# Optimization experiments

Hardware: AMD Instinct MI355X
Metric: run time of the kernel (lower is better)

Reference implementation:

```python
import jax, jax.numpy as jnp
import numpy as np

H_SIZE = 1024
N_HEADS = 16
D_K = H_SIZE // N_HEADS


def setup_inputs() -> dict:
    key = jax.random.key(0)
    ks = jax.random.split(key, 12)
    s = 1.0 / np.sqrt(H_SIZE)
    inp = {
        "x": jax.random.normal(ks[0], (2, 2048, H_SIZE), dtype=jnp.float32),
        "Wq": jax.random.uniform(ks[1], (H_SIZE, H_SIZE), minval=-s, maxval=s),
        "bq": jax.random.uniform(ks[2], (H_SIZE,), minval=-s, maxval=s),
        "Wk": jax.random.uniform(ks[3], (H_SIZE, H_SIZE), minval=-s, maxval=s),
        "bk": jax.random.uniform(ks[4], (H_SIZE,), minval=-s, maxval=s),
        "Wv": jax.random.uniform(ks[5], (H_SIZE, H_SIZE), minval=-s, maxval=s),
        "bv": jax.random.uniform(ks[6], (H_SIZE,), minval=-s, maxval=s),
        "Wo": jax.random.uniform(ks[7], (H_SIZE, H_SIZE), minval=-s, maxval=s),
        "bo": jax.random.uniform(ks[8], (H_SIZE,), minval=-s, maxval=s),
        "ln_gamma": jnp.ones((H_SIZE,), dtype=jnp.float32),
        "ln_beta": jnp.zeros((H_SIZE,), dtype=jnp.float32),
    }
    return inp


def reference(x, Wq, bq, Wk, bk, Wv, bv, Wo, bo, ln_gamma, ln_beta):
    B, L, H = x.shape
    residual = x
    # QKV projections -> [B, n_heads, L, d_k]
    def proj(W, b):
        return (x @ W.T + b).reshape(B, L, N_HEADS, D_K).transpose(0, 2, 1, 3)
    q = proj(Wq, bq)
    k = proj(Wk, bk)
    v = proj(Wv, bv)
    # scaled dot-product attention (dropout = identity in eval mode)
    scores = jnp.einsum("bhqd,bhkd->bhqk", q, k) / jnp.sqrt(jnp.float32(D_K))
    attn = jax.nn.softmax(scores, axis=-1)
    out = jnp.einsum("bhqk,bhkd->bhqd", attn, v)
    out = out.transpose(0, 2, 1, 3).reshape(B, L, H)
    out = out @ Wo.T + bo
    # residual + LayerNorm
    y = out + residual
    mu = jnp.mean(y, axis=-1, keepdims=True)
    var = jnp.var(y, axis=-1, keepdims=True)
    y = (y - mu) / jnp.sqrt(var + 1e-5) * ln_gamma + ln_beta
    return y
```

## Files before the change

### kernel.cpp

```cpp
#include <hip/hip_runtime.h>

#define H_SIZE 1024
#define N_HEADS 16
#define D_K 64
#define SEQ 2048
#define BATCH 2
#define M_TOT 4096

typedef __bf16 __attribute__((ext_vector_type(8))) bf16_8;
typedef float __attribute__((ext_vector_type(4))) f32x4;
typedef float __attribute__((ext_vector_type(16))) f32x16;
typedef int __attribute__((ext_vector_type(4))) int4v;

__device__ __forceinline__ ushort f2bf(float f) {
    unsigned int u = __float_as_uint(f);
    unsigned int r = (u + 0x7FFFu + ((u >> 16) & 1u)) >> 16;
    return (ushort)r;
}

__device__ __forceinline__ unsigned int cvtpk(float lo, float hi) {
    unsigned int r;
    asm("v_cvt_pk_bf16_f32 %0, %1, %2" : "=v"(r) : "v"(lo), "v"(hi));
    return r;
}

__device__ __forceinline__ void gld16(void* lds, const void* g) {
    __builtin_amdgcn_global_load_lds(
        (const __attribute__((address_space(1))) unsigned int*)g,
        (__attribute__((address_space(3))) unsigned int*)lds, 16, 0, 0);
}

__global__ __launch_bounds__(256) void cast_all_kernel(
    const float* __restrict__ x, const float* __restrict__ wq, const float* __restrict__ wk,
    const float* __restrict__ wv, const float* __restrict__ wo,
    ushort* __restrict__ xb, ushort* __restrict__ wqb, ushort* __restrict__ wkb,
    ushort* __restrict__ wvb, ushort* __restrict__ wob) {
    int i = blockIdx.x * 256 + threadIdx.x;
    const float* src;
    ushort* dst;
    int off;
    if (i < 1048576) {
        src = x; dst = xb; off = i;
    } else {
        int j = i - 1048576;
        int w = j >> 18;
        off = j & 262143;
        src = (w == 0) ? wq : (w == 1) ? wk : (w == 2) ? wv : wo;
        dst = (w == 0) ? wqb : (w == 1) ? wkb : (w == 2) ? wvb : wob;
    }
    float4 v = ((const float4*)src)[off];
    ushort4 o;
    o.x = f2bf(v.x); o.y = f2bf(v.y); o.z = f2bf(v.z); o.w = f2bf(v.w);
    ((ushort4*)dst)[off] = o;
}

__global__ __launch_bounds__(256) void gemm_qkv(
    const ushort* __restrict__ A, const ushort* __restrict__ wq,
    const ushort* __restrict__ wk, const ushort* __restrict__ wv,
    const float* __restrict__ bq, const float* __restrict__ bk, const float* __restrict__ bv,
    ushort* __restrict__ Qb, ushort* __restrict__ Kb, ushort* __restrict__ Vtb) {
    constexpr int LDST = 40;
    __shared__ ushort As[2][128 * LDST];
    __shared__ ushort Bs[2][128 * LDST];
    const int tid = threadIdx.x;
    const int lane = tid & 63, wid = tid >> 6;
    const int wr = wid >> 1, wc = wid & 1;
    const int hi = lane >> 4, lo = lane & 15;
    const int bm0 = blockIdx.x * 128;
    const int t3 = blockIdx.y >> 3;
    const int bn0 = (blockIdx.y & 7) * 128;
    const ushort* Bw = (t3 == 0) ? wq : (t3 == 1) ? wk : wv;
    const float* bias = (t3 == 0) ? bq : (t3 == 1) ? bk : bv;

    f32x4 acc[4][4] = {};

    const int r = tid >> 1, c0 = (tid & 1) * 16;
    const ushort* ga = A + (size_t)(bm0 + r) * H_SIZE + c0;
    const ushort* gb = Bw + (size_t)(bn0 + r) * H_SIZE + c0;

    int4v a0, a1, b0, b1;
#define LOADR(kt)                                  \
    {                                              \
        a0 = *(const int4v*)(ga + (kt));           \
        a1 = *(const int4v*)(ga + (kt) + 8);       \
        b0 = *(const int4v*)(gb + (kt));           \
        b1 = *(const int4v*)(gb + (kt) + 8);       \
    }
#define STORER(bb)                                 \
    {                                              \
        ushort* sa = &As[bb][r * LDST + c0];       \
        *(int4v*)sa = a0; *(int4v*)(sa + 8) = a1;  \
        ushort* sb = &Bs[bb][r * LDST + c0];       \
        *(int4v*)sb = b0; *(int4v*)(sb + 8) = b1;  \
    }

    LOADR(0);
    STORER(0);
    __syncthreads();
    int cur = 0;
    constexpr int NT = H_SIZE / 32;
    for (int t = 0; t < NT; t++) {
        if (t + 1 < NT) LOADR((t + 1) * 32);
        {
            bf16_8 af[4], bfv[4];
            const ushort* pa = &As[cur][(wr * 64 + lo) * LDST + hi * 8];
            const ushort* pb = &Bs[cur][(wc * 64 + lo) * LDST + hi * 8];
#pragma unroll
            for (int i = 0; i < 4; i++) af[i] = *(const bf16_8*)(pa + i * 16 * LDST);
#pragma unroll
            for (int i = 0; i < 4; i++) bfv[i] = *(const bf16_8*)(pb + i * 16 * LDST);
#pragma unroll
            for (int mi = 0; mi < 4; mi++)
#pragma unroll
                for (int ni = 0; ni < 4; ni++)
                    acc[mi][ni] = __builtin_amdgcn_mfma_f32_16x16x32_bf16(
                        af[mi], bfv[ni], acc[mi][ni], 0, 0, 0);
        }
        if (t + 1 < NT) {
            STORER(cur ^ 1);
            __syncthreads();
        }
        cur ^= 1;
    }
#undef LOADR
#undef STORER

#pragma unroll
    for (int mi = 0; mi < 4; mi++) {
#pragma unroll
        for (int ni = 0; ni < 4; ni++) {
            const int row0 = bm0 + wr * 64 + mi * 16 + hi * 4;
            const int col = bn0 + wc * 64 + ni * 16 + lo;
            const float bv = bias[col];
            const int h = col >> 6, dk = col & 63;
            if (t3 == 2) {
                const int b = row0 >> 11, l0 = row0 & 2047;
                const int lsw0 = (l0 & ~63) | ((((l0 >> 3) & 7) ^ (dk & 7)) << 3) | (l0 & 7);
                ushort4 o;
                o.x = f2bf(acc[mi][ni][0] + bv);
                o.y = f2bf(acc[mi][ni][1] + bv);
                o.z = f2bf(acc[mi][ni][2] + bv);
                o.w = f2bf(acc[mi][ni][3] + bv);
                *(ushort4*)&Vtb[((size_t)(b * N_HEADS + h) * D_K + dk) * SEQ + lsw0] = o;
            } else {
#pragma unroll
                for (int rr = 0; rr < 4; rr++) {
                    const int m = row0 + rr;
                    const int b = m >> 11, l = m & 2047;
                    float val = acc[mi][ni][rr] + bv;
                    if (t3 == 0) {
                        Qb[((size_t)(b * N_HEADS + h) * SEQ + l) * D_K + dk] = f2bf(val * 0.125f);
                    } else {
                        int dks = (((dk >> 3) ^ (l & 7)) << 3) | (dk & 7);
                        Kb[((size_t)(b * N_HEADS + h) * SEQ + l) * D_K + dks] = f2bf(val);
                    }
                }
            }
        }
    }
}

__global__ __launch_bounds__(256) void gemm_o(const ushort* __restrict__ A,
                                              const ushort* __restrict__ Bw,
                                              const float* __restrict__ bias,
                                              const float* __restrict__ resid,
                                              float* __restrict__ outp) {
    constexpr int LDST = 40;
    __shared__ ushort As[2][128 * LDST];
    __shared__ ushort Bs[2][64 * LDST];
    const int tid = threadIdx.x;
    const int lane = tid & 63, wid = tid >> 6;
    const int wr = wid >> 1, wc = wid & 1;
    const int hi = lane >> 4, lo = lane & 15;
    const int bm0 = blockIdx.x * 128, bn0 = blockIdx.y * 64;

    f32x4 acc[4][2] = {};

    const int ra = tid >> 1, ca0 = (tid & 1) * 16;
    const int rb = tid >> 2, cb0 = (tid & 3) * 8;
    const ushort* ga = A + (size_t)(bm0 + ra) * H_SIZE + ca0;
    const ushort* gb = Bw + (size_t)(bn0 + rb) * H_SIZE + cb0;

    int4v a0, a1, b0;
#define LOADR(kt)                                  \
    {                                              \
        a0 = *(const int4v*)(ga + (kt));           \
        a1 = *(const int4v*)(ga + (kt) + 8);       \
        b0 = *(const int4v*)(gb + (kt));           \
    }
#define STORER(bb)                                 \
    {                                              \
        ushort* sa = &As[bb][ra * LDST + ca0];     \
        *(int4v*)sa = a0; *(int4v*)(sa + 8) = a1;  \
        *(int4v*)&Bs[bb][rb * LDST + cb0] = b0;    \
    }

    LOADR(0);
    STORER(0);
    __syncthreads();
    int cur = 0;
    constexpr int NT = H_SIZE / 32;
    for (int t = 0; t < NT; t++) {
        if (t + 1 < NT) LOADR((t + 1) * 32);
        {
            bf16_8 af[4], bfv[2];
            const ushort* pa = &As[cur][(wr * 64 + lo) * LDST + hi * 8];
            const ushort* pb = &Bs[cur][(wc * 32 + lo) * LDST + hi * 8];
#pragma unroll
            for (int i = 0; i < 4; i++) af[i] = *(const bf16_8*)(pa + i * 16 * LDST);
#pragma unroll
            for (int i = 0; i < 2; i++) bfv[i] = *(const bf16_8*)(pb + i * 16 * LDST);
#pragma unroll
            for (int mi = 0; mi < 4; mi++)
#pragma unroll
                for (int ni = 0; ni < 2; ni++)
                    acc[mi][ni] = __builtin_amdgcn_mfma_f32_16x16x32_bf16(
                        af[mi], bfv[ni], acc[mi][ni], 0, 0, 0);
        }
        if (t + 1 < NT) {
            STORER(cur ^ 1);
            __syncthreads();
        }
        cur ^= 1;
    }
#undef LOADR
#undef STORER

#pragma unroll
    for (int mi = 0; mi < 4; mi++) {
#pragma unroll
        for (int ni = 0; ni < 2; ni++) {
            const int row0 = bm0 + wr * 64 + mi * 16 + hi * 4;
            const int col = bn0 + wc * 32 + ni * 16 + lo;
            const float bv = bias[col];
#pragma unroll
            for (int rr = 0; rr < 4; rr++) {
                const int m = row0 + rr;
                outp[(size_t)m * H_SIZE + col] =
                    acc[mi][ni][rr] + bv + resid[(size_t)m * H_SIZE + col];
            }
        }
    }
}

__global__ __launch_bounds__(256) void attn_kernel(const ushort* __restrict__ Q,
                                                   const ushort* __restrict__ Ksw,
                                                   const ushort* __restrict__ Vsw,
                                                   ushort* __restrict__ Out) {
    __shared__ ushort Ks[2][64 * 64];
    __shared__ ushort Vs[2][64 * 64];
    __shared__ float lsum_lds[4][32];
    const int lane = threadIdx.x & 63, wid = threadIdx.x >> 6;
    const int h32 = lane >> 5, q32 = lane & 31;
    const int bh = blockIdx.y;
    const int q0w = blockIdx.x * 128 + wid * 32;
    const ushort* Qh = Q + (size_t)bh * SEQ * D_K;
    const ushort* Kp = Ksw + (size_t)bh * SEQ * D_K;
    const ushort* Vp = Vsw + (size_t)bh * D_K * SEQ;

    bf16_8 qf[4];
#pragma unroll
    for (int tt = 0; tt < 4; tt++)
        qf[tt] = *(const bf16_8*)(Qh + (size_t)(q0w + q32) * D_K + tt * 16 + h32 * 8);

    f32x16 oacc0 = {}, oacc1 = {};
    float ls = 0.f;

    const int koff = wid * 2048 + lane * 16;
    const int vrow = wid * 16 + (lane >> 3);
    const int vseg = (lane & 7) * 16;

#define STAGE(bb, kt)                                                             \
    {                                                                             \
        const char* kg = (const char*)(Kp + (size_t)(kt) * D_K);                  \
        char* kl = (char*)&Ks[bb][0];                                             \
        gld16(kl + koff, kg + koff);                                              \
        gld16(kl + koff + 1024, kg + koff + 1024);                                \
        char* vl = (char*)&Vs[bb][0];                                             \
        gld16(vl + vrow * 128 + vseg,                                             \
              (const char*)(Vp + (size_t)vrow * SEQ + (kt)) + vseg);              \
        gld16(vl + (vrow + 8) * 128 + vseg,                                       \
              (const char*)(Vp + (size_t)(vrow + 8) * SEQ + (kt)) + vseg);        \
    }

    STAGE(0, 0);
    __syncthreads();
    int buf = 0;
    for (int t = 0; t < SEQ / 64; t++) {
        if (t + 1 < SEQ / 64) STAGE(buf ^ 1, (t + 1) * 64);
        const ushort* kb = &Ks[buf][0];
        const ushort* vb = &Vs[buf][0];
#pragma unroll
        for (int kh = 0; kh < 2; kh++) {
            f32x16 st = {};
            const int krow = kh * 32 + q32;
#pragma unroll
            for (int tt = 0; tt < 4; tt++) {
                int sg = ((2 * tt + h32) ^ (krow & 7));
                bf16_8 kf = *(const bf16_8*)(kb + krow * 64 + sg * 8);
                st = __builtin_amdgcn_mfma_f32_32x32x16_bf16(kf, qf[tt], st, 0, 0, 0);
            }
            float p[16];
#pragma unroll
            for (int rr = 0; rr < 16; rr++) p[rr] = __expf(st[rr]);
            float partial = 0.f;
#pragma unroll
            for (int rr = 0; rr < 16; rr++) partial += p[rr];
            ls += partial + __shfl_xor(partial, 32);

            union { unsigned int w[4]; bf16_8 v; } pf0, pf1;
#pragma unroll
            for (int i = 0; i < 2; i++) {
                unsigned int a = cvtpk(p[2 * i], p[2 * i + 1]);
                unsigned int b = cvtpk(p[4 + 2 * i], p[4 + 2 * i + 1]);
                asm volatile("v_permlane32_swap_b32 %0, %1" : "+v"(a), "+v"(b));
                pf0.w[i] = a; pf0.w[2 + i] = b;
                unsigned int c = cvtpk(p[8 + 2 * i], p[8 + 2 * i + 1]);
                unsigned int d = cvtpk(p[12 + 2 * i], p[12 + 2 * i + 1]);
                asm volatile("v_permlane32_swap_b32 %0, %1" : "+v"(c), "+v"(d));
                pf1.w[i] = c; pf1.w[2 + i] = d;
            }

            {
                const int vr0 = q32;
                int sg0 = ((4 * kh + h32) ^ (vr0 & 7));
                int sg1 = ((4 * kh + 2 + h32) ^ (vr0 & 7));
                bf16_8 vf0 = *(const bf16_8*)(vb + vr0 * 64 + sg0 * 8);
                bf16_8 vf1 = *(const bf16_8*)(vb + vr0 * 64 + sg1 * 8);
                oacc0 = __builtin_amdgcn_mfma_f32_32x32x16_bf16(pf0.v, vf0, oacc0, 0, 0, 0);
                oacc0 = __builtin_amdgcn_mfma_f32_32x32x16_bf16(pf1.v, vf1, oacc0, 0, 0, 0);
            }
            {
                const int vr1 = 32 + q32;
                int sg0 = ((4 * kh + h32) ^ (vr1 & 7));
                int sg1 = ((4 * kh + 2 + h32) ^ (vr1 & 7));
                bf16_8 vf0 = *(const bf16_8*)(vb + vr1 * 64 + sg0 * 8);
                bf16_8 vf1 = *(const bf16_8*)(vb + vr1 * 64 + sg1 * 8);
                oacc1 = __builtin_amdgcn_mfma_f32_32x32x16_bf16(pf0.v, vf0, oacc1, 0, 0, 0);
                oacc1 = __builtin_amdgcn_mfma_f32_32x32x16_bf16(pf1.v, vf1, oacc1, 0, 0, 0);
            }
        }
        __syncthreads();
        buf ^= 1;
    }
#undef STAGE

    if (lane < 32) lsum_lds[wid][q32] = 1.0f / ls;
    const int b = bh >> 4, h = bh & 15;
#pragma unroll
    for (int rr = 0; rr < 16; rr++) {
        const int qloc = (rr & 3) + 8 * (rr >> 2) + 4 * h32;
        const float inv = lsum_lds[wid][qloc];
        const int l = q0w + qloc;
        ushort* orow = Out + ((size_t)(b * SEQ + l)) * H_SIZE + h * 64;
        orow[q32] = f2bf(oacc0[rr] * inv);
        orow[32 + q32] = f2bf(oacc1[rr] * inv);
    }
}

__global__ __launch_bounds__(256) void ln_kernel(float* __restrict__ y,
                                                 const float* __restrict__ gamma,
                                                 const float* __restrict__ beta) {
    const int row = blockIdx.x;
    float4* p = (float4*)(y + (size_t)row * H_SIZE);
    float4 v = p[threadIdx.x];
    float s = v.x + v.y + v.z + v.w;
    float s2 = v.x * v.x + v.y * v.y + v.z * v.z + v.w * v.w;
#pragma unroll
    for (int off = 1; off < 64; off <<= 1) {
        s += __shfl_xor(s, off);
        s2 += __shfl_xor(s2, off);
    }
    __shared__ float ss[4], ss2[4];
    const int wid = threadIdx.x >> 6, lane = threadIdx.x & 63;
    if (lane == 0) { ss[wid] = s; ss2[wid] = s2; }
    __syncthreads();
    s = ss[0] + ss[1] + ss[2] + ss[3];
    s2 = ss2[0] + ss2[1] + ss2[2] + ss2[3];
    const float mean = s * (1.0f / H_SIZE);
    const float var = s2 * (1.0f / H_SIZE) - mean * mean;
    const float rstd = rsqrtf(var + 1e-5f);
    const float4 g = ((const float4*)gamma)[threadIdx.x];
    const float4 bt = ((const float4*)beta)[threadIdx.x];
    float4 o;
    o.x = (v.x - mean) * rstd * g.x + bt.x;
    o.y = (v.y - mean) * rstd * g.y + bt.y;
    o.z = (v.z - mean) * rstd * g.z + bt.z;
    o.w = (v.w - mean) * rstd * g.w + bt.w;
    p[threadIdx.x] = o;
}

extern "C" void kernel_launch(void* const* d_in, const int* in_sizes, int n_in,
                              void* d_out, int out_size, void* d_ws, size_t ws_size,
                              hipStream_t stream) {
    const float* x = (const float*)d_in[0];
    const float* Wq = (const float*)d_in[1];
    const float* bq = (const float*)d_in[2];
    const float* Wk = (const float*)d_in[3];
    const float* bk = (const float*)d_in[4];
    const float* Wv = (const float*)d_in[5];
    const float* bv = (const float*)d_in[6];
    const float* Wo = (const float*)d_in[7];
    const float* bo = (const float*)d_in[8];
    const float* gamma = (const float*)d_in[9];
    const float* beta = (const float*)d_in[10];

    char* ws = (char*)d_ws;
    ushort* xb  = (ushort*)(ws);
    ushort* wqb = (ushort*)(ws + (8u << 20));
    ushort* wkb = (ushort*)(ws + (10u << 20));
    ushort* wvb = (ushort*)(ws + (12u << 20));
    ushort* wob = (ushort*)(ws + (14u << 20));
    ushort* Qb  = (ushort*)(ws + (16u << 20));
    ushort* Kb  = (ushort*)(ws + (24u << 20));
    ushort* Vtb = (ushort*)(ws + (32u << 20));
    ushort* Ao  = (ushort*)(ws + (40u << 20));

    cast_all_kernel<<<8192, 256, 0, stream>>>(x, Wq, Wk, Wv, Wo, xb, wqb, wkb, wvb, wob);

    dim3 gq(M_TOT / 128, 24);
    gemm_qkv<<<gq, 256, 0, stream>>>(xb, wqb, wkb, wvb, bq, bk, bv, Qb, Kb, Vtb);

    dim3 g2(SEQ / 128, BATCH * N_HEADS);
    attn_kernel<<<g2, 256, 0, stream>>>(Qb, Kb, Vtb, Ao);

    dim3 go(M_TOT / 128, H_SIZE / 64);
    gemm_o<<<go, 256, 0, stream>>>(Ao, wob, bo, x, (float*)d_out);

    ln_kernel<<<M_TOT, 256, 0, stream>>>((float*)d_out, gamma, beta);
}
```

Measured before the change: 135.6 us.

## Use direct global-to-LDS loads with BK=64 in projection GEMMs, exp2 softmax

The QKV and output projection GEMMs now stage tiles with global_load_lds (direct global-to-LDS DMA) instead of register round-trips. The K tile per step grows from 32 to 64, which halves the number of barriers. The LDS tiles are unpadded, with a 64-element row stride, and the GEMM fragment reads are not swizzled, so these reads may hit LDS bank conflicts. The attention kernel replaces __expf with raw v_exp_f32 (exp2), with log2(e) folded into the Q scale, and changes the K/V swizzle to a two-level XOR pattern, which the producer and consumer must both apply consistently.

```diff
diff --git a/kernel.cpp b/kernel.cpp
--- a/kernel.cpp
+++ b/kernel.cpp
@@ -12,6 +12,8 @@
 typedef float __attribute__((ext_vector_type(16))) f32x16;
 typedef int __attribute__((ext_vector_type(4))) int4v;
 
+#define SWZ(r) ((((r) & 7) ^ (((r) >> 3) & 7)))
+
 __device__ __forceinline__ ushort f2bf(float f) {
     unsigned int u = __float_as_uint(f);
     unsigned int r = (u + 0x7FFFu + ((u >> 16) & 1u)) >> 16;
@@ -21,6 +23,12 @@
 __device__ __forceinline__ unsigned int cvtpk(float lo, float hi) {
     unsigned int r;
     asm("v_cvt_pk_bf16_f32 %0, %1, %2" : "=v"(r) : "v"(lo), "v"(hi));
+    return r;
+}
+
+__device__ __forceinline__ float exp2_raw(float x) {
+    float r;
+    asm("v_exp_f32 %0, %1" : "=v"(r) : "v"(x));
     return r;
 }
 
@@ -59,9 +67,8 @@
     const ushort* __restrict__ wk, const ushort* __restrict__ wv,
     const float* __restrict__ bq, const float* __restrict__ bk, const float* __restrict__ bv,
     ushort* __restrict__ Qb, ushort* __restrict__ Kb, ushort* __restrict__ Vtb) {
-    constexpr int LDST = 40;
-    __shared__ ushort As[2][128 * LDST];
-    __shared__ ushort Bs[2][128 * LDST];
+    __shared__ ushort As[2][128 * 64];
+    __shared__ ushort Bs[2][128 * 64];
     const int tid = threadIdx.x;
     const int lane = tid & 63, wid = tid >> 6;
     const int wr = wid >> 1, wc = wid & 1;
@@ -74,41 +81,41 @@
 
     f32x4 acc[4][4] = {};
 
-    const int r = tid >> 1, c0 = (tid & 1) * 16;
-    const ushort* ga = A + (size_t)(bm0 + r) * H_SIZE + c0;
-    const ushort* gb = Bw + (size_t)(bn0 + r) * H_SIZE + c0;
-
-    int4v a0, a1, b0, b1;
-#define LOADR(kt)                                  \
-    {                                              \
-        a0 = *(const int4v*)(ga + (kt));           \
-        a1 = *(const int4v*)(ga + (kt) + 8);       \
-        b0 = *(const int4v*)(gb + (kt));           \
-        b1 = *(const int4v*)(gb + (kt) + 8);       \
-    }
-#define STORER(bb)                                 \
-    {                                              \
-        ushort* sa = &As[bb][r * LDST + c0];       \
-        *(int4v*)sa = a0; *(int4v*)(sa + 8) = a1;  \
-        ushort* sb = &Bs[bb][r * LDST + c0];       \
-        *(int4v*)sb = b0; *(int4v*)(sb + 8) = b1;  \
-    }
-
-    LOADR(0);
-    STORER(0);
+    const int srow = tid >> 3;
+    const int sseg = (tid & 7) * 8;
+    const ushort* gaB = A + (size_t)(bm0 + srow) * H_SIZE + sseg;
+    const ushort* gbB = Bw + (size_t)(bn0 + srow) * H_SIZE + sseg;
+    const int ldsOff = tid * 16;
+
+#define STAGE(bb, kt)                                                     \
+    {                                                                     \
+        char* la = (char*)&As[bb][0] + ldsOff;                            \
+        char* lb = (char*)&Bs[bb][0] + ldsOff;                            \
+        gld16(la, gaB + (kt));                                            \
+        gld16(la + 4096, gaB + 32 * H_SIZE + (kt));                       \
+        gld16(la + 8192, gaB + 64 * H_SIZE + (kt));                       \
+        gld16(la + 12288, gaB + 96 * H_SIZE + (kt));                      \
+        gld16(lb, gbB + (kt));                                            \
+        gld16(lb + 4096, gbB + 32 * H_SIZE + (kt));                       \
+        gld16(lb + 8192, gbB + 64 * H_SIZE + (kt));                       \
+        gld16(lb + 12288, gbB + 96 * H_SIZE + (kt));                      \
+    }
+
+    STAGE(0, 0);
     __syncthreads();
     int cur = 0;
-    constexpr int NT = H_SIZE / 32;
+    constexpr int NT = H_SIZE / 64;
     for (int t = 0; t < NT; t++) {
-        if (t + 1 < NT) LOADR((t + 1) * 32);
-        {
+        if (t + 1 < NT) STAGE(cur ^ 1, (t + 1) * 64);
+#pragma unroll
+        for (int kk = 0; kk < 64; kk += 32) {
             bf16_8 af[4], bfv[4];
-            const ushort* pa = &As[cur][(wr * 64 + lo) * LDST + hi * 8];
-            const ushort* pb = &Bs[cur][(wc * 64 + lo) * LDST + hi * 8];
-#pragma unroll
-            for (int i = 0; i < 4; i++) af[i] = *(const bf16_8*)(pa + i * 16 * LDST);
-#pragma unroll
-            for (int i = 0; i < 4; i++) bfv[i] = *(const bf16_8*)(pb + i * 16 * LDST);
+            const ushort* pa = &As[cur][(wr * 64 + lo) * 64 + kk + hi * 8];
+            const ushort* pb = &Bs[cur][(wc * 64 + lo) * 64 + kk + hi * 8];
+#pragma unroll
+            for (int i = 0; i < 4; i++) af[i] = *(const bf16_8*)(pa + i * 16 * 64);
+#pragma unroll
+            for (int i = 0; i < 4; i++) bfv[i] = *(const bf16_8*)(pb + i * 16 * 64);
 #pragma unroll
             for (int mi = 0; mi < 4; mi++)
 #pragma unroll
@@ -116,14 +123,10 @@
                     acc[mi][ni] = __builtin_amdgcn_mfma_f32_16x16x32_bf16(
                         af[mi], bfv[ni], acc[mi][ni], 0, 0, 0);
         }
-        if (t + 1 < NT) {
-            STORER(cur ^ 1);
-            __syncthreads();
-        }
+        __syncthreads();
         cur ^= 1;
     }
-#undef LOADR
-#undef STORER
+#undef STAGE
 
 #pragma unroll
     for (int mi = 0; mi < 4; mi++) {
@@ -135,7 +138,7 @@
             const int h = col >> 6, dk = col & 63;
             if (t3 == 2) {
                 const int b = row0 >> 11, l0 = row0 & 2047;
-                const int lsw0 = (l0 & ~63) | ((((l0 >> 3) & 7) ^ (dk & 7)) << 3) | (l0 & 7);
+                const int lsw0 = (l0 & ~63) | (((((l0 >> 3) & 7) ^ SWZ(dk)) & 7) << 3) | (l0 & 7);
                 ushort4 o;
                 o.x = f2bf(acc[mi][ni][0] + bv);
                 o.y = f2bf(acc[mi][ni][1] + bv);
@@ -149,9 +152,10 @@
                     const int b = m >> 11, l = m & 2047;
                     float val = acc[mi][ni][rr] + bv;
                     if (t3 == 0) {
-                        Qb[((size_t)(b * N_HEADS + h) * SEQ + l) * D_K + dk] = f2bf(val * 0.125f);
+                        Qb[((size_t)(b * N_HEADS + h) * SEQ + l) * D_K + dk] =
+                            f2bf(val * 0.18033688f);
                     } else {
-                        int dks = (((dk >> 3) ^ (l & 7)) << 3) | (dk & 7);
+                        int dks = ((((dk >> 3) ^ SWZ(l & 63)) & 7) << 3) | (dk & 7);
                         Kb[((size_t)(b * N_HEADS + h) * SEQ + l) * D_K + dks] = f2bf(val);
                     }
                 }
@@ -165,9 +169,8 @@
                                               const float* __restrict__ bias,
                                               const float* __restrict__ resid,
                                               float* __restrict__ outp) {
-    constexpr int LDST = 40;
-    __shared__ ushort As[2][128 * LDST];
-    __shared__ ushort Bs[2][64 * LDST];
+    __shared__ ushort As[2][128 * 64];
+    __shared__ ushort Bs[2][64 * 64];
     const int tid = threadIdx.x;
     const int lane = tid & 63, wid = tid >> 6;
     const int wr = wid >> 1, wc = wid & 1;
@@ -176,40 +179,39 @@
 
     f32x4 acc[4][2] = {};
 
-    const int ra = tid >> 1, ca0 = (tid & 1) * 16;
-    const int rb = tid >> 2, cb0 = (tid & 3) * 8;
-    const ushort* ga = A + (size_t)(bm0 + ra) * H_SIZE + ca0;
-    const ushort* gb = Bw + (size_t)(bn0 + rb) * H_SIZE + cb0;
-
-    int4v a0, a1, b0;
-#define LOADR(kt)                                  \
-    {                                              \
-        a0 = *(const int4v*)(ga + (kt));           \
-        a1 = *(const int4v*)(ga + (kt) + 8);       \
-        b0 = *(const int4v*)(gb + (kt));           \
-    }
-#define STORER(bb)                                 \
-    {                                              \
-        ushort* sa = &As[bb][ra * LDST + ca0];     \
-        *(int4v*)sa = a0; *(int4v*)(sa + 8) = a1;  \
-        *(int4v*)&Bs[bb][rb * LDST + cb0] = b0;    \
-    }
-
-    LOADR(0);
-    STORER(0);
+    const int srow = tid >> 3;
+    const int sseg = (tid & 7) * 8;
+    const ushort* gaB = A + (size_t)(bm0 + srow) * H_SIZE + sseg;
+    const ushort* gbB = Bw + (size_t)(bn0 + srow) * H_SIZE + sseg;
+    const int ldsOff = tid * 16;
+
+#define STAGE(bb, kt)                                                     \
+    {                                                                     \
+        char* la = (char*)&As[bb][0] + ldsOff;                            \
+        char* lb = (char*)&Bs[bb][0] + ldsOff;                            \
+        gld16(la, gaB + (kt));                                            \
+        gld16(la + 4096, gaB + 32 * H_SIZE + (kt));                       \
+        gld16(la + 8192, gaB + 64 * H_SIZE + (kt));                       \
+        gld16(la + 12288, gaB + 96 * H_SIZE + (kt));                      \
+        gld16(lb, gbB + (kt));                                            \
+        gld16(lb + 4096, gbB + 32 * H_SIZE + (kt));                       \
+    }
+
+    STAGE(0, 0);
     __syncthreads();
     int cur = 0;
-    constexpr int NT = H_SIZE / 32;
+    constexpr int NT = H_SIZE / 64;
     for (int t = 0; t < NT; t++) {
-        if (t + 1 < NT) LOADR((t + 1) * 32);
-        {
+        if (t + 1 < NT) STAGE(cur ^ 1, (t + 1) * 64);
+#pragma unroll
+        for (int kk = 0; kk < 64; kk += 32) {
             bf16_8 af[4], bfv[2];
-            const ushort* pa = &As[cur][(wr * 64 + lo) * LDST + hi * 8];
-            const ushort* pb = &Bs[cur][(wc * 32 + lo) * LDST + hi * 8];
-#pragma unroll
-            for (int i = 0; i < 4; i++) af[i] = *(const bf16_8*)(pa + i * 16 * LDST);
-#pragma unroll
-            for (int i = 0; i < 2; i++) bfv[i] = *(const bf16_8*)(pb + i * 16 * LDST);
+            const ushort* pa = &As[cur][(wr * 64 + lo) * 64 + kk + hi * 8];
+            const ushort* pb = &Bs[cur][(wc * 32 + lo) * 64 + kk + hi * 8];
+#pragma unroll
+            for (int i = 0; i < 4; i++) af[i] = *(const bf16_8*)(pa + i * 16 * 64);
+#pragma unroll
+            for (int i = 0; i < 2; i++) bfv[i] = *(const bf16_8*)(pb + i * 16 * 64);
 #pragma unroll
             for (int mi = 0; mi < 4; mi++)
 #pragma unroll
@@ -217,14 +219,10 @@
                     acc[mi][ni] = __builtin_amdgcn_mfma_f32_16x16x32_bf16(
                         af[mi], bfv[ni], acc[mi][ni], 0, 0, 0);
         }
-        if (t + 1 < NT) {
-            STORER(cur ^ 1);
-            __syncthreads();
-        }
+        __syncthreads();
         cur ^= 1;
     }
-#undef LOADR
-#undef STORER
+#undef STAGE
 
 #pragma unroll
     for (int mi = 0; mi < 4; mi++) {
@@ -296,13 +294,13 @@
             const int krow = kh * 32 + q32;
 #pragma unroll
             for (int tt = 0; tt < 4; tt++) {
-                int sg = ((2 * tt + h32) ^ (krow & 7));
+                int sg = (2 * tt + h32) ^ SWZ(krow);
                 bf16_8 kf = *(const bf16_8*)(kb + krow * 64 + sg * 8);
                 st = __builtin_amdgcn_mfma_f32_32x32x16_bf16(kf, qf[tt], st, 0, 0, 0);
             }
             float p[16];
 #pragma unroll
-            for (int rr = 0; rr < 16; rr++) p[rr] = __expf(st[rr]);
+            for (int rr = 0; rr < 16; rr++) p[rr] = exp2_raw(st[rr]);
             float partial = 0.f;
 #pragma unroll
             for (int rr = 0; rr < 16; rr++) partial += p[rr];
@@ -323,8 +321,8 @@
 
             {
                 const int vr0 = q32;
-                int sg0 = ((4 * kh + h32) ^ (vr0 & 7));
-                int sg1 = ((4 * kh + 2 + h32) ^ (vr0 & 7));
+                int sg0 = (4 * kh + h32) ^ SWZ(vr0);
+                int sg1 = (4 * kh + 2 + h32) ^ SWZ(vr0);
                 bf16_8 vf0 = *(const bf16_8*)(vb + vr0 * 64 + sg0 * 8);
                 bf16_8 vf1 = *(const bf16_8*)(vb + vr0 * 64 + sg1 * 8);
                 oacc0 = __builtin_amdgcn_mfma_f32_32x32x16_bf16(pf0.v, vf0, oacc0, 0, 0, 0);
@@ -332,8 +330,8 @@
             }
             {
                 const int vr1 = 32 + q32;
-                int sg0 = ((4 * kh + h32) ^ (vr1 & 7));
-                int sg1 = ((4 * kh + 2 + h32) ^ (vr1 & 7));
+                int sg0 = (4 * kh + h32) ^ SWZ(vr1);
+                int sg1 = (4 * kh + 2 + h32) ^ SWZ(vr1);
                 bf16_8 vf0 = *(const bf16_8*)(vb + vr1 * 64 + sg0 * 8);
                 bf16_8 vf1 = *(const bf16_8*)(vb + vr1 * 64 + sg1 * 8);
                 oacc1 = __builtin_amdgcn_mfma_f32_32x32x16_bf16(pf0.v, vf0, oacc1, 0, 0, 0);
```

After: 155.4 us. 14.6% more time.
